# Optimization experiments

Measured on AMD Instinct MI355X. Metric: run time of the kernel, lower is better.

The kernel has to match this reference:

```python
import jax, jax.numpy as jnp
import numpy as np

T = 10
EPS = 1e-05

def setup_inputs() -> dict:
    key = jax.random.key(0)
    k1, k2 = jax.random.split(key)
    B, C, H, W = 128, 64, 56, 56
    X = jax.random.normal(k1, (B, C, H, W), dtype=jnp.float32)
    beta = jnp.zeros((C,), dtype=jnp.float32)
    return {"X": X, "beta": beta}


def reference(X, beta):
    # Training-path of BWItnBlock.forward (grad enabled branch of iter_norm_batch)
    B, C, H, W = X.shape
    d = C                      # n_channels, num_groups g = 1
    m = B * H * W
    # x = X.transpose(0,1).view(g, d, -1)  -> [d, m] with g=1
    x = jnp.transpose(X, (1, 0, 2, 3)).reshape(d, m)
    mean = jnp.mean(x, axis=1, keepdims=True)          # [d, 1]
    xc = x - mean                                      # [d, m]
    I = jnp.eye(d, dtype=X.dtype)
    # Sigma = eps*I + xc xc^T / m
    Sigma = EPS * I + (xc @ xc.T) / m                  # [d, d]
    # fix_cov: multiply off-diagonal by 0.9, diagonal by 1.0
    fix = 0.9 + 0.1 * I
    Sigma = Sigma * fix
    rTr = 1.0 / jnp.trace(Sigma)                       # scalar (sum(Sigma * I))
    Sigma_N = Sigma * rTr
    # Newton-Schulz iterations for inverse sqrt: P <- 1.5 P - 0.5 P^3 Sigma_N
    P = I
    for _ in range(T):
        P = 1.5 * P - 0.5 * ((P @ P @ P) @ Sigma_N)
    wm = P * jnp.sqrt(rTr)                             # whitening matrix [d, d]
    xn = wm @ xc                                       # [d, m]
    X_hat = jnp.transpose(xn.reshape(C, B, H, W), (1, 0, 2, 3))
    X_hat = X_hat + beta.reshape(1, C, 1, 1)
    return X_hat
```

## Files before the change

kernel.cpp:

```cpp
#include <hip/hip_runtime.h>

#define CH 64
#define HW 3136
#define MTOT 401408
#define TPX 128

typedef __attribute__((ext_vector_type(8))) short short8;
typedef __attribute__((ext_vector_type(4))) float f32x4;
typedef __attribute__((ext_vector_type(4))) unsigned int u32x4;

__device__ __forceinline__ void split8(const float4 a, const float4 b,
                                       short8& hi, short8& lo, float& ssum){
  const float f[8] = {a.x,a.y,a.z,a.w, b.x,b.y,b.z,b.w};
  u32x4 hp, lp;
#pragma unroll
  for (int j=0;j<4;++j){
    const unsigned int b0 = __float_as_uint(f[2*j]);
    const unsigned int b1 = __float_as_uint(f[2*j+1]);
    hp[j] = (b0 >> 16) | (b1 & 0xFFFF0000u);
    const float h0 = __uint_as_float(b0 & 0xFFFF0000u);
    const float h1 = __uint_as_float(b1 & 0xFFFF0000u);
    const unsigned int l0 = __float_as_uint(f[2*j]   - h0);
    const unsigned int l1 = __float_as_uint(f[2*j+1] - h1);
    lp[j] = (l0 >> 16) | (l1 & 0xFFFF0000u);
  }
  hi = __builtin_bit_cast(short8, hp);
  lo = __builtin_bit_cast(short8, lp);
  ssum += ((f[0]+f[1])+(f[2]+f[3])) + ((f[4]+f[5])+(f[6]+f[7]));
}

__global__ __launch_bounds__(256) void k1_cov(const float* __restrict__ X,
                                              float* __restrict__ SR){
  constexpr int RG[10] = {0,1,1,2,2,2,3,3,3,3};
  constexpr int CG[10] = {0,0,1,0,1,2,0,1,2,3};
  __shared__ __align__(16) float buf[2][64*TPX];
  __shared__ float chs[64];

  const int t   = threadIdx.x;
  const int wid = __builtin_amdgcn_readfirstlane(t >> 6);
  const int l   = t & 63;
  const int lr  = l & 15;
  const int q   = l >> 4;
  const int bid = blockIdx.x;
  const int t0  = bid*6 + (bid < 64 ? bid : 64);
  const int nt  = (bid < 64) ? 7 : 6;

  f32x4 acc[10];
#pragma unroll
  for (int bi=0; bi<10; ++bi) acc[bi] = (f32x4){0.f,0.f,0.f,0.f};
  float sums[4] = {0.f,0.f,0.f,0.f};

  auto stage = [&](int tg, float* dst){
    const unsigned mbase = (unsigned)tg * TPX;
#pragma unroll
    for (int j=0;j<8;++j){
      const int r  = 16*wid + 2*j + (l>>5);
      const int cb = (l&31) ^ (r&7);
      const unsigned m  = mbase + 4*cb;
      const unsigned b  = m / HW;
      const unsigned hw = m - b*HW;
      const float* src = X + (size_t)b*(CH*HW) + (size_t)r*HW + hw;
      __builtin_amdgcn_global_load_lds(
        (const __attribute__((address_space(1))) unsigned int*)src,
        (__attribute__((address_space(3))) unsigned int*)(dst + (16*wid + 2*j)*TPX),
        16, 0, 0);
    }
  };

  stage(t0, buf[0]);
  int pb = 0;
  for (int tl=0; tl<nt; ++tl){
    if (tl+1 < nt){
      stage(t0+tl+1, buf[pb^1]);
      asm volatile("s_waitcnt vmcnt(8)" ::: "memory");
    } else {
      asm volatile("s_waitcnt vmcnt(0)" ::: "memory");
    }
    __builtin_amdgcn_sched_barrier(0);
    asm volatile("s_barrier" ::: "memory");
    const char* bp = (const char*)buf[pb];
    short8 fh[4], fl[4];
#pragma unroll
    for (int g=0; g<4; ++g){
      const int r   = 16*g + lr;
      const int sw  = r & 7;
      const int cb0 = 8*wid + 2*q;
      const float4 v0 = *(const float4*)(bp + r*512 + 16*((cb0+0)^sw));
      const float4 v1 = *(const float4*)(bp + r*512 + 16*((cb0+1)^sw));
      split8(v0, v1, fh[g], fl[g], sums[g]);
    }
#pragma unroll
    for (int bi=0; bi<10; ++bi){
      acc[bi] = __builtin_amdgcn_mfma_f32_16x16x32_bf16(fh[RG[bi]], fh[CG[bi]], acc[bi], 0,0,0);
      acc[bi] = __builtin_amdgcn_mfma_f32_16x16x32_bf16(fh[RG[bi]], fl[CG[bi]], acc[bi], 0,0,0);
      acc[bi] = __builtin_amdgcn_mfma_f32_16x16x32_bf16(fl[RG[bi]], fh[CG[bi]], acc[bi], 0,0,0);
    }
    asm volatile("s_barrier" ::: "memory");
    pb ^= 1;
  }

#pragma unroll
  for (int g=0; g<4; ++g){
    sums[g] += __shfl_xor(sums[g], 16);
    sums[g] += __shfl_xor(sums[g], 32);
  }

  float* red = &buf[0][0];
  for (int w=0; w<4; ++w){
    if (wid == w){
#pragma unroll
      for (int bi=0; bi<10; ++bi){
        const int row0 = RG[bi]*16 + 4*q;
        const int col  = CG[bi]*16 + lr;
#pragma unroll
        for (int r=0; r<4; ++r){
          float* d = &red[(row0+r)*64 + col];
          if (w==0) *d = acc[bi][r]; else *d += acc[bi][r];
        }
      }
      if (l < 16){
#pragma unroll
        for (int g=0; g<4; ++g){
          if (w==0) chs[g*16+l] = sums[g]; else chs[g*16+l] += sums[g];
        }
      }
    }
    __syncthreads();
  }

#pragma unroll
  for (int bi=0; bi<10; ++bi){
    const int r = RG[bi]*16 + (t>>4);
    const int c = CG[bi]*16 + (t&15);
    unsafeAtomicAdd(&SR[r*64+c], red[r*64+c]);
  }
  if (t < 64) unsafeAtomicAdd(&SR[4096+t], chs[t]);
}

__device__ __forceinline__ void mm_AtB(const float* a, const float* b, float* out,
                                       float alpha, const float* aff, float beta_){
  const int t = threadIdx.x;
  const int c2 = 2*(t & 31);
  const int r0 = 8*(t >> 5);
  float acc[8][2];
#pragma unroll
  for (int i=0;i<8;++i){ acc[i][0]=0.f; acc[i][1]=0.f; }
  for (int k=0;k<64;++k){
    const float2 bv = *(const float2*)&b[k*64 + c2];
    const float4 a0 = *(const float4*)&a[k*64 + r0];
    const float4 a1 = *(const float4*)&a[k*64 + r0 + 4];
    const float av[8] = {a0.x,a0.y,a0.z,a0.w, a1.x,a1.y,a1.z,a1.w};
#pragma unroll
    for (int i=0;i<8;++i){ acc[i][0] += av[i]*bv.x; acc[i][1] += av[i]*bv.y; }
  }
  float res[8][2];
#pragma unroll
  for (int i=0;i<8;++i){
    float f0 = alpha*acc[i][0], f1 = alpha*acc[i][1];
    if (aff){ f0 += beta_*aff[(r0+i)*64 + c2]; f1 += beta_*aff[(r0+i)*64 + c2 + 1]; }
    res[i][0]=f0; res[i][1]=f1;
  }
  __syncthreads();
#pragma unroll
  for (int i=0;i<8;++i){
    float2 o2; o2.x = res[i][0]; o2.y = res[i][1];
    *(float2*)&out[(r0+i)*64 + c2] = o2;
  }
  __syncthreads();
}

__global__ __launch_bounds__(256) void k2_wm(const float* __restrict__ SR,
                                             const float* __restrict__ beta,
                                             float* __restrict__ WM,
                                             float* __restrict__ OFS){
  __shared__ __align__(16) float bufE[4096];
  __shared__ __align__(16) float bufA[4096];
  __shared__ __align__(16) float bufB[4096];
  __shared__ float meanv[64];
  __shared__ float scal[2];
  const int t = threadIdx.x;
  const float inv_m = 1.f/(float)MTOT;
  if (t < 64) meanv[t] = SR[4096 + t]*inv_m;
  __syncthreads();
  for (int idx=t; idx<4096; idx+=256){
    const int r = idx >> 6, c = idx & 63;
    const int src = ((r >> 4) >= (c >> 4)) ? idx : (c*64 + r);
    const float cov = SR[src]*inv_m - meanv[r]*meanv[c];
    bufE[idx] = (r==c) ? (cov + 1e-5f - 1.f) : 0.9f*cov;
  }
  __syncthreads();
  float n2 = 0.f, tr = 0.f;
  for (int idx=t; idx<4096; idx+=256){
    const float e = bufE[idx];
    n2 += e*e;
    if ((idx >> 6) == (idx & 63)) tr += e;
  }
  bufA[t] = n2; bufB[t] = tr;
  __syncthreads();
  if (t < 64){
    bufA[t] = bufA[t]+bufA[t+64]+bufA[t+128]+bufA[t+192];
    bufB[t] = bufB[t]+bufB[t+64]+bufB[t+128]+bufB[t+192];
  }
  __syncthreads();
  if (t == 0){
    float s1=0.f, s2=0.f;
    for (int i=0;i<64;++i){ s1 += bufA[i]; s2 += bufB[i]; }
    scal[0] = s1; scal[1] = s2;
  }
  __syncthreads();
  const float frob2 = scal[0];
  const float trE   = scal[1];
  float wscale = 1.f;
  const float* wmLds;
  if (frob2 < 0.04f){
    mm_AtB(bufE, bufE, bufA, 1.f, nullptr, 0.f);
    mm_AtB(bufA, bufE, bufB, 1.f, nullptr, 0.f);
    for (int idx=t; idx<4096; idx+=256){
      const int r = idx >> 6, c = idx & 63;
      bufB[idx] = ((r==c)?1.f:0.f) - 0.5f*bufE[idx] + 0.375f*bufA[idx] - 0.3125f*bufB[idx];
    }
    mm_AtB(bufA, bufA, bufE, 1.f, nullptr, 0.f);
    for (int idx=t; idx<4096; idx+=256)
      bufB[idx] += 0.2734375f*bufE[idx];
    wmLds = bufB;
  } else {
    const float rTr = 1.f/(trE + 64.f);
    for (int idx=t; idx<4096; idx+=256){
      const int r = idx >> 6, c = idx & 63;
      bufE[idx] = (bufE[idx] + ((r==c)?1.f:0.f))*rTr;
      bufA[idx] = (r==c)?1.f:0.f;
    }
    __syncthreads();
    for (int it=0; it<10; ++it){
      mm_AtB(bufA, bufE, bufB, 1.f, nullptr, 0.f);
      mm_AtB(bufA, bufB, bufB, 1.f, nullptr, 0.f);
      mm_AtB(bufA, bufB, bufA, -0.5f, bufA, 1.5f);
    }
    wscale = sqrtf(rTr);
    wmLds = bufA;
  }
  __syncthreads();
  for (int idx=t; idx<4096; idx+=256) WM[idx] = wmLds[idx]*wscale;
  if (t < 64){
    float d = 0.f;
    for (int j=0;j<64;++j) d += wmLds[t*64 + j]*meanv[j];
    OFS[t] = beta[t] - d*wscale;
  }
}

__global__ __launch_bounds__(256) void k3_apply(const float* __restrict__ X,
                                                const float* __restrict__ WM,
                                                const float* __restrict__ OFS,
                                                float* __restrict__ out){
  __shared__ __align__(16) float tile[64*TPX];
  const int t   = threadIdx.x;
  const int wid = __builtin_amdgcn_readfirstlane(t >> 6);
  const int l   = t & 63;
  const int lr  = l & 15;
  const int q   = l >> 4;

  {
    const unsigned mbase = (unsigned)blockIdx.x * TPX;
#pragma unroll
    for (int j=0;j<8;++j){
      const int r = 16*wid + 2*j + (l>>5);
      const unsigned pxs = 4*(l&31);
      const unsigned m  = mbase + (pxs ^ (((r>>3)&1u)<<4));
      const unsigned b  = m / HW;
      const unsigned hw = m - b*HW;
      const float* src = X + (size_t)b*(CH*HW) + (size_t)r*HW + hw;
      __builtin_amdgcn_global_load_lds(
        (const __attribute__((address_space(1))) unsigned int*)src,
        (__attribute__((address_space(3))) unsigned int*)(tile + (16*wid + 2*j)*TPX),
        16, 0, 0);
    }
  }

  short8 ah[4][2], al[4][2];
  float dummy = 0.f;
#pragma unroll
  for (int cb=0; cb<4; ++cb)
#pragma unroll
    for (int ks=0; ks<2; ++ks){
      const float* wp = WM + (16*cb + lr)*64 + ks*32 + q*8;
      const float4 w0 = *(const float4*)wp;
      const float4 w1 = *(const float4*)(wp + 4);
      split8(w0, w1, ah[cb][ks], al[cb][ks], dummy);
    }

  asm volatile("s_waitcnt vmcnt(0)" ::: "memory");
  __syncthreads();

  f32x4 acc[4][2];
#pragma unroll
  for (int cb=0; cb<4; ++cb)
#pragma unroll
    for (int pk=0; pk<2; ++pk) acc[cb][pk] = (f32x4){0.f,0.f,0.f,0.f};

#pragma unroll
  for (int ks=0; ks<2; ++ks){
    short8 bh[2], bl[2];
#pragma unroll
    for (int pk=0; pk<2; ++pk){
      const int ch0 = ks*32 + q*8;
      const int pxl = 32*wid + 16*pk + lr;
      const int pxs = pxl ^ ((q&1)<<4);
      const float* rp = tile + ch0*TPX + pxs;
      float f[8];
#pragma unroll
      for (int j=0;j<8;++j) f[j] = rp[j*TPX];
      const float4 v0 = {f[0],f[1],f[2],f[3]};
      const float4 v1 = {f[4],f[5],f[6],f[7]};
      split8(v0, v1, bh[pk], bl[pk], dummy);
    }
#pragma unroll
    for (int cb=0; cb<4; ++cb)
#pragma unroll
      for (int pk=0; pk<2; ++pk){
        acc[cb][pk] = __builtin_amdgcn_mfma_f32_16x16x32_bf16(ah[cb][ks], bh[pk], acc[cb][pk], 0,0,0);
        acc[cb][pk] = __builtin_amdgcn_mfma_f32_16x16x32_bf16(ah[cb][ks], bl[pk], acc[cb][pk], 0,0,0);
        acc[cb][pk] = __builtin_amdgcn_mfma_f32_16x16x32_bf16(al[cb][ks], bh[pk], acc[cb][pk], 0,0,0);
      }
  }
  __syncthreads();

#pragma unroll
  for (int cb=0; cb<4; ++cb)
#pragma unroll
    for (int pk=0; pk<2; ++pk)
#pragma unroll
      for (int r=0; r<4; ++r){
        const int ch = 16*cb + 4*q + r;
        const int px = (32*wid + 16*pk + lr) ^ (((ch>>2)&1)<<4);
        tile[ch*TPX + px] = acc[cb][pk][r];
      }
  __syncthreads();

  {
    const int c0 = 16*wid;
    const unsigned P2 = (unsigned)blockIdx.x*TPX + 2*l;
    const unsigned b2 = P2 / HW;
    const unsigned hw2 = P2 - b2*HW;
    float* ob = out + (size_t)b2*(CH*HW) + hw2;
#pragma unroll
    for (int i=0;i<16;++i){
      const int c = c0 + i;
      const int px = (2*l) ^ (((c>>2)&1)<<4);
      const float2 v = *(const float2*)&tile[c*TPX + px];
      const float o = OFS[c];
      float2 pkv; pkv.x = v.x + o; pkv.y = v.y + o;
      *(float2*)(ob + (size_t)c*HW) = pkv;
    }
  }
}

extern "C" void kernel_launch(void* const* d_in, const int* in_sizes, int n_in,
                              void* d_out, int out_size, void* d_ws, size_t ws_size,
                              hipStream_t stream){
  const float* X    = (const float*)d_in[0];
  const float* beta = (const float*)d_in[1];
  float* out = (float*)d_out;
  float* ws  = (float*)d_ws;
  float* SR  = ws;
  float* WM  = ws + 4160;
  float* OFS = WM + 4096;
  hipMemsetAsync(SR, 0, 4160*sizeof(float), stream);
  hipLaunchKernelGGL(k1_cov,   dim3(512),  dim3(256), 0, stream, X, SR);
  hipLaunchKernelGGL(k2_wm,    dim3(1),    dim3(256), 0, stream, SR, beta, WM, OFS);
  hipLaunchKernelGGL(k3_apply, dim3(3136), dim3(256), 0, stream, X, WM, OFS, out);
}
```

Before: 228.6 us.

## Split covariance pass into many small blocks with partial buffers and a reduction kernel

The covariance kernel goes from 512 persistent double-buffered blocks to 1568 blocks that each handle two tiles with single-buffered, synchronous staging. Each block now writes its 64x64 partial (upper blocks plus channel sums) to a workspace buffer instead of adding atomically into the shared result. A new reduction kernel sums these partials and does a few atomics per element. This trades the old load/compute overlap for more parallelism and less atomic contention, at the cost of about 16 MB of extra partial traffic and one more kernel launch.

```diff
diff --git a/kernel.cpp b/kernel.cpp
--- a/kernel.cpp
+++ b/kernel.cpp
@@ -4,6 +4,8 @@
 #define HW 3136
 #define MTOT 401408
 #define TPX 128
+#define K1_NBLK 1568
+#define NPART 1568
 
 typedef __attribute__((ext_vector_type(8))) short short8;
 typedef __attribute__((ext_vector_type(4))) float f32x4;
@@ -30,10 +32,10 @@
 }
 
 __global__ __launch_bounds__(256) void k1_cov(const float* __restrict__ X,
-                                              float* __restrict__ SR){
+                                              float* __restrict__ PART){
   constexpr int RG[10] = {0,1,1,2,2,2,3,3,3,3};
   constexpr int CG[10] = {0,0,1,0,1,2,0,1,2,3};
-  __shared__ __align__(16) float buf[2][64*TPX];
+  __shared__ __align__(16) float tile[64*TPX];
   __shared__ float chs[64];
 
   const int t   = threadIdx.x;
@@ -41,44 +43,34 @@
   const int l   = t & 63;
   const int lr  = l & 15;
   const int q   = l >> 4;
-  const int bid = blockIdx.x;
-  const int t0  = bid*6 + (bid < 64 ? bid : 64);
-  const int nt  = (bid < 64) ? 7 : 6;
 
   f32x4 acc[10];
 #pragma unroll
   for (int bi=0; bi<10; ++bi) acc[bi] = (f32x4){0.f,0.f,0.f,0.f};
   float sums[4] = {0.f,0.f,0.f,0.f};
 
-  auto stage = [&](int tg, float* dst){
-    const unsigned mbase = (unsigned)tg * TPX;
-#pragma unroll
-    for (int j=0;j<8;++j){
-      const int r  = 16*wid + 2*j + (l>>5);
-      const int cb = (l&31) ^ (r&7);
-      const unsigned m  = mbase + 4*cb;
-      const unsigned b  = m / HW;
-      const unsigned hw = m - b*HW;
-      const float* src = X + (size_t)b*(CH*HW) + (size_t)r*HW + hw;
-      __builtin_amdgcn_global_load_lds(
-        (const __attribute__((address_space(1))) unsigned int*)src,
-        (__attribute__((address_space(3))) unsigned int*)(dst + (16*wid + 2*j)*TPX),
-        16, 0, 0);
-    }
-  };
-
-  stage(t0, buf[0]);
-  int pb = 0;
-  for (int tl=0; tl<nt; ++tl){
-    if (tl+1 < nt){
-      stage(t0+tl+1, buf[pb^1]);
-      asm volatile("s_waitcnt vmcnt(8)" ::: "memory");
-    } else {
-      asm volatile("s_waitcnt vmcnt(0)" ::: "memory");
-    }
-    __builtin_amdgcn_sched_barrier(0);
-    asm volatile("s_barrier" ::: "memory");
-    const char* bp = (const char*)buf[pb];
+#pragma unroll
+  for (int tl=0; tl<2; ++tl){
+    {
+      const unsigned mbase = (unsigned)(blockIdx.x*2 + tl) * TPX;
+#pragma unroll
+      for (int j=0;j<8;++j){
+        const int r  = 16*wid + 2*j + (l>>5);
+        const int cb = (l&31) ^ (r&7);
+        const unsigned m  = mbase + 4*cb;
+        const unsigned b  = m / HW;
+        const unsigned hw = m - b*HW;
+        const float* src = X + (size_t)b*(CH*HW) + (size_t)r*HW + hw;
+        __builtin_amdgcn_global_load_lds(
+          (const __attribute__((address_space(1))) unsigned int*)src,
+          (__attribute__((address_space(3))) unsigned int*)(tile + (16*wid + 2*j)*TPX),
+          16, 0, 0);
+      }
+    }
+    asm volatile("s_waitcnt vmcnt(0)" ::: "memory");
+    __syncthreads();
+
+    const char* bp = (const char*)tile;
     short8 fh[4], fl[4];
 #pragma unroll
     for (int g=0; g<4; ++g){
@@ -89,14 +81,14 @@
       const float4 v1 = *(const float4*)(bp + r*512 + 16*((cb0+1)^sw));
       split8(v0, v1, fh[g], fl[g], sums[g]);
     }
+    __syncthreads();
+
 #pragma unroll
     for (int bi=0; bi<10; ++bi){
       acc[bi] = __builtin_amdgcn_mfma_f32_16x16x32_bf16(fh[RG[bi]], fh[CG[bi]], acc[bi], 0,0,0);
       acc[bi] = __builtin_amdgcn_mfma_f32_16x16x32_bf16(fh[RG[bi]], fl[CG[bi]], acc[bi], 0,0,0);
       acc[bi] = __builtin_amdgcn_mfma_f32_16x16x32_bf16(fl[RG[bi]], fh[CG[bi]], acc[bi], 0,0,0);
     }
-    asm volatile("s_barrier" ::: "memory");
-    pb ^= 1;
   }
 
 #pragma unroll
@@ -105,7 +97,7 @@
     sums[g] += __shfl_xor(sums[g], 32);
   }
 
-  float* red = &buf[0][0];
+  float* red = &tile[0];
   for (int w=0; w<4; ++w){
     if (wid == w){
 #pragma unroll
@@ -128,13 +120,42 @@
     __syncthreads();
   }
 
+  float* pb = PART + (size_t)blockIdx.x * 2624;
 #pragma unroll
   for (int bi=0; bi<10; ++bi){
     const int r = RG[bi]*16 + (t>>4);
     const int c = CG[bi]*16 + (t&15);
-    unsafeAtomicAdd(&SR[r*64+c], red[r*64+c]);
-  }
-  if (t < 64) unsafeAtomicAdd(&SR[4096+t], chs[t]);
+    pb[bi*256 + t] = red[r*64 + c];
+  }
+  if (t < 64) pb[2560 + t] = chs[t];
+}
+
+__global__ __launch_bounds__(256) void k1_red(const float* __restrict__ PART,
+                                              float* __restrict__ SR){
+  constexpr int RG[10] = {0,1,1,2,2,2,3,3,3,3};
+  constexpr int CG[10] = {0,0,1,0,1,2,0,1,2,3};
+  __shared__ float lds[256];
+  const int t = threadIdx.x;
+  const int l = t & 63;
+  const int w = t >> 6;
+  const int j  = blockIdx.x*64 + l;
+  const int p0 = blockIdx.y*196 + w*49;
+  float s = 0.f;
+#pragma unroll 7
+  for (int i=0;i<49;++i) s += PART[(size_t)(p0+i)*2624 + j];
+  lds[t] = s;
+  __syncthreads();
+  if (w == 0){
+    const float tot = lds[l] + lds[l+64] + lds[l+128] + lds[l+192];
+    int idx;
+    if (j < 2560){
+      const int bi = j >> 8, tt = j & 255;
+      idx = (RG[bi]*16 + (tt>>4))*64 + CG[bi]*16 + (tt&15);
+    } else {
+      idx = 4096 + (j - 2560);
+    }
+    unsafeAtomicAdd(&SR[idx], tot);
+  }
 }
 
 __device__ __forceinline__ void mm_AtB(const float* a, const float* b, float* out,
@@ -361,11 +382,13 @@
   const float* beta = (const float*)d_in[1];
   float* out = (float*)d_out;
   float* ws  = (float*)d_ws;
-  float* SR  = ws;
-  float* WM  = ws + 4160;
-  float* OFS = WM + 4096;
+  float* SR   = ws;
+  float* WM   = ws + 4160;
+  float* OFS  = WM + 4096;
+  float* PART = ws + 8384;
   hipMemsetAsync(SR, 0, 4160*sizeof(float), stream);
-  hipLaunchKernelGGL(k1_cov,   dim3(512),  dim3(256), 0, stream, X, SR);
-  hipLaunchKernelGGL(k2_wm,    dim3(1),    dim3(256), 0, stream, SR, beta, WM, OFS);
-  hipLaunchKernelGGL(k3_apply, dim3(3136), dim3(256), 0, stream, X, WM, OFS, out);
-}
+  hipLaunchKernelGGL(k1_cov, dim3(K1_NBLK),  dim3(256), 0, stream, X, PART);
+  hipLaunchKernelGGL(k1_red, dim3(41, 8),    dim3(256), 0, stream, PART, SR);
+  hipLaunchKernelGGL(k2_wm,  dim3(1),        dim3(256), 0, stream, SR, beta, WM, OFS);
+  hipLaunchKernelGGL(k3_apply, dim3(3136),   dim3(256), 0, stream, X, WM, OFS, out);
+}
```

After: 231.0 us. About the same (+1.0%).
